# Performance work log

Hardware: AMD Instinct MI355X
Metric: run time of the kernel (lower is better)

## Reference

```python
import jax, jax.numpy as jnp
import numpy as np

N, C, H, W = 8, 256, 56, 56
DEPTH, HEADS, NWIN, TOPK, MLPR = 4, 8, 7, 4, 4
EPS = 1e-6


def setup_inputs() -> dict:
    key = jax.random.key(0)
    ks = jax.random.split(key, 16)
    s = 0.02
    return {
        'x': jax.random.normal(ks[0], (N, C, H, W), jnp.float32),
        'ln1_w': jnp.ones((DEPTH, C), jnp.float32),
        'ln1_b': jnp.zeros((DEPTH, C), jnp.float32),
        'qkv_w': jax.random.normal(ks[1], (DEPTH, C, 3 * C), jnp.float32) * s,
        'qkv_b': jnp.zeros((DEPTH, 3 * C), jnp.float32),
        'lepe_w': jax.random.normal(ks[2], (DEPTH, C, 1, 5, 5), jnp.float32) * s,
        'lepe_b': jnp.zeros((DEPTH, C), jnp.float32),
        'wo_w': jax.random.normal(ks[3], (DEPTH, C, C), jnp.float32) * s,
        'wo_b': jnp.zeros((DEPTH, C), jnp.float32),
        'ln2_w': jnp.ones((DEPTH, C), jnp.float32),
        'ln2_b': jnp.zeros((DEPTH, C), jnp.float32),
        'mlp1_w': jax.random.normal(ks[4], (DEPTH, C, MLPR * C), jnp.float32) * s,
        'mlp1_b': jnp.zeros((DEPTH, MLPR * C), jnp.float32),
        'mlp2_w': jax.random.normal(ks[5], (DEPTH, MLPR * C, C), jnp.float32) * s,
        'mlp2_b': jnp.zeros((DEPTH, C), jnp.float32),
        'cse1_w': jax.random.normal(ks[6], (C // 16, C), jnp.float32) * s,
        'cse1_b': jnp.zeros((C // 16,), jnp.float32),
        'cse2_w': jax.random.normal(ks[7], (C, C // 16), jnp.float32) * s,
        'cse2_b': jnp.zeros((C,), jnp.float32),
        'sse_w': jax.random.normal(ks[8], (C, C), jnp.float32) * s,
        'sse_b': jnp.zeros((C,), jnp.float32),
        'conv_w': jax.random.normal(ks[9], (C, C, 3, 3), jnp.float32) * s,
        'conv_b': jnp.zeros((C,), jnp.float32),
    }


def _layernorm(x, w, b):
    mu = x.mean(-1, keepdims=True)
    var = ((x - mu) ** 2).mean(-1, keepdims=True)
    return (x - mu) * jax.lax.rsqrt(var + EPS) * w + b


def _dwconv5(x_nchw, k, b):
    # depthwise 5x5 conv, padding 2; k: (C,1,5,5)
    y = jax.lax.conv_general_dilated(
        x_nchw, k, (1, 1), [(2, 2), (2, 2)],
        dimension_numbers=('NCHW', 'OIHW', 'NCHW'), feature_group_count=C)
    return y + b[None, :, None, None]


def _bra(xn, qkv_w, qkv_b, lepe_w, lepe_b, wo_w, wo_b):
    # Bi-level routing attention on NHWC input (already layer-normed).
    j = NWIN; hh = H // j; ww = W // j; p2 = j * j; hw = hh * ww
    scale = C ** -0.5  # qk_dim == dim
    qkv = xn @ qkv_w + qkv_b                      # [N,H,W,3C]
    q, k, v = jnp.split(qkv, 3, axis=-1)

    def to_regions(t):  # [N,H,W,C] -> [N,p2,hw,C]
        return t.reshape(N, j, hh, j, ww, C).transpose(0, 1, 3, 2, 4, 5).reshape(N, p2, hw, C)

    q_pix, k_pix, v_pix = to_regions(q), to_regions(k), to_regions(v)
    # region-level descriptors (routing is detached in original: diff_routing=False)
    q_win = jax.lax.stop_gradient(q_pix.mean(2))  # [N,p2,C]
    k_win = jax.lax.stop_gradient(k_pix.mean(2))
    logits = jnp.einsum('npc,nqc->npq', q_win * scale, k_win)
    _, idx = jax.lax.top_k(logits, TOPK)          # [N,p2,TOPK]; routing weights unused (mul_weight='none')
    bidx = jnp.arange(N)[:, None, None]
    k_sel = k_pix[bidx, idx]                      # [N,p2,TOPK,hw,C] irregular gather
    v_sel = v_pix[bidx, idx]
    m = HEADS; cd = C // m
    qh = q_pix.reshape(N, p2, hw, m, cd)
    kh = k_sel.reshape(N, p2, TOPK * hw, m, cd)
    vh = v_sel.reshape(N, p2, TOPK * hw, m, cd)
    attn = jnp.einsum('npqmc,npkmc->npmqk', qh * scale, kh)
    attn = jax.nn.softmax(attn, axis=-1)
    out = jnp.einsum('npmqk,npkmc->npqmc', attn, vh).reshape(N, p2, hw, C)
    out = out.reshape(N, j, j, hh, ww, C).transpose(0, 1, 3, 2, 4, 5).reshape(N, H, W, C)
    lepe = _dwconv5(v.transpose(0, 3, 1, 2), lepe_w, lepe_b).transpose(0, 2, 3, 1)
    return (out + lepe) @ wo_w + wo_b


def _forward(x, ln1_w, ln1_b, qkv_w, qkv_b, lepe_w, lepe_b, wo_w, wo_b,
             ln2_w, ln2_b, mlp1_w, mlp1_b, mlp2_w, mlp2_b,
             cse1_w, cse1_b, cse2_w, cse2_b, sse_w, sse_b, conv_w, conv_b):
    xh = x.transpose(0, 2, 3, 1)  # NCHW -> NHWC
    for i in range(DEPTH):
        xh = xh + _bra(_layernorm(xh, ln1_w[i], ln1_b[i]),
                       qkv_w[i], qkv_b[i], lepe_w[i], lepe_b[i], wo_w[i], wo_b[i])
        xn = _layernorm(xh, ln2_w[i], ln2_b[i])
        h = jax.nn.gelu(xn @ mlp1_w[i] + mlp1_b[i], approximate=False)
        xh = xh + h @ mlp2_w[i] + mlp2_b[i]
    y = xh.transpose(0, 3, 1, 2)  # NHWC -> NCHW
    # SCSE gating
    pooled = y.mean((2, 3))  # [N,C] adaptive avg pool
    c = jax.nn.relu(pooled @ cse1_w.T + cse1_b)
    c = jax.nn.sigmoid(c @ cse2_w.T + cse2_b)  # [N,C]
    s = jax.nn.sigmoid(jnp.einsum('nchw,oc->nohw', y, sse_w) + sse_b[None, :, None, None])
    y = y * c[:, :, None, None] + y * s
    # final 3x3 conv, padding 1
    y = jax.lax.conv_general_dilated(
        y, conv_w, (1, 1), [(1, 1), (1, 1)],
        dimension_numbers=('NCHW', 'OIHW', 'NCHW')) + conv_b[None, :, None, None]
    return y


def reference(x, ln1_w, ln1_b, qkv_w, qkv_b, lepe_w, lepe_b, wo_w, wo_b,
              ln2_w, ln2_b, mlp1_w, mlp1_b, mlp2_w, mlp2_b,
              cse1_w, cse1_b, cse2_w, cse2_b, sse_w, sse_b, conv_w, conv_b):
    return _forward(x, ln1_w, ln1_b, qkv_w, qkv_b, lepe_w, lepe_b, wo_w, wo_b,
                    ln2_w, ln2_b, mlp1_w, mlp1_b, mlp2_w, mlp2_b,
                    cse1_w, cse1_b, cse2_w, cse2_b, sse_w, sse_b, conv_w, conv_b)
```

## Files before the change

kernel.cpp:

```cpp
#include <hip/hip_runtime.h>

#define PIX 25088
#define NB 8
#define HH 56
#define WW 56
#define CC 256
#define P2 49
#define TOPKN 4

typedef short s16x8 __attribute__((ext_vector_type(8)));
typedef float f32x4 __attribute__((ext_vector_type(4)));

__device__ __forceinline__ float gelu_f(float v){
    return 0.5f*v*(1.0f+erff(v*0.70710678118654752f));
}
__device__ __forceinline__ float sigmoid_f(float v){
    return 1.0f/(1.0f+__expf(-v));
}
__device__ __forceinline__ unsigned short f2bf(float f){
    union { float f; unsigned u; } x; x.f = f;
    unsigned r = x.u + 0x7fffu + ((x.u >> 16) & 1u);
    return (unsigned short)(r >> 16);
}
__device__ __forceinline__ float bf2f(unsigned short u){
    union { unsigned u; float f; } x; x.u = ((unsigned)u) << 16; return x.f;
}
__device__ __forceinline__ void gload_lds16(const void* g, void* l){
    __builtin_amdgcn_global_load_lds((const __attribute__((address_space(1))) void*)g,
                                     (__attribute__((address_space(3))) void*)l, 16, 0, 0);
}

__global__ __launch_bounds__(1024) void nchw_to_nhwc(const float* __restrict__ in, float* __restrict__ out){
    __shared__ float t[32][33];
    int pb = blockIdx.x;
    int n  = pb / 98;
    int p0 = (pb % 98) * 32;
    int c0 = blockIdx.y * 32;
    int tx = threadIdx.x, ty = threadIdx.y;
    t[ty][tx] = in[(size_t)(n*CC + c0+ty)*3136 + p0 + tx];
    __syncthreads();
    out[(size_t)(n*3136 + p0 + ty)*CC + c0 + tx] = t[tx][ty];
}

__global__ __launch_bounds__(1024) void wtrans(const float* __restrict__ in, unsigned short* __restrict__ out,
                                               int K, int N){
    int layer = blockIdx.z;
    in  += (size_t)layer*K*N;
    out += (size_t)layer*K*N;
    __shared__ float t[32][33];
    int n0 = blockIdx.x*32, k0 = blockIdx.y*32;
    t[threadIdx.y][threadIdx.x] = in[(size_t)(k0+threadIdx.y)*N + n0 + threadIdx.x];
    __syncthreads();
    out[(size_t)(n0+threadIdx.y)*K + k0 + threadIdx.x] = f2bf(t[threadIdx.x][threadIdx.y]);
}

__global__ __launch_bounds__(256) void tobf16(const float* __restrict__ in, unsigned short* __restrict__ out, int n){
    int i = blockIdx.x*256 + threadIdx.x;
    if(i < n) out[i] = f2bf(in[i]);
}

__global__ __launch_bounds__(256) void convw_reorder(const float* __restrict__ in, unsigned short* __restrict__ out){
    int idx = blockIdx.x*256 + threadIdx.x;
    if(idx >= 256*256*9) return;
    int o = idx / (256*9); int rem = idx % (256*9); int c = rem/9; int t = rem%9;
    out[(size_t)t*65536 + o*256 + c] = f2bf(in[idx]);
}

__global__ __launch_bounds__(256) void ln_bf16(const float* __restrict__ x, const float* __restrict__ w,
                                               const float* __restrict__ b, unsigned short* __restrict__ y){
    int row = blockIdx.x*4 + (threadIdx.x >> 6);
    int lane = threadIdx.x & 63;
    const float4 v = *reinterpret_cast<const float4*>(&x[(size_t)row*CC + lane*4]);
    float s = v.x + v.y + v.z + v.w;
    #pragma unroll
    for(int off=32; off>0; off>>=1) s += __shfl_xor(s, off);
    float mu = s*(1.0f/CC);
    float d0=v.x-mu, d1=v.y-mu, d2=v.z-mu, d3=v.w-mu;
    float sq = d0*d0 + d1*d1 + d2*d2 + d3*d3;
    #pragma unroll
    for(int off=32; off>0; off>>=1) sq += __shfl_xor(sq, off);
    float rs = rsqrtf(sq*(1.0f/CC) + 1e-6f);
    const float4 wv = *reinterpret_cast<const float4*>(&w[lane*4]);
    const float4 bv = *reinterpret_cast<const float4*>(&b[lane*4]);
    ushort4 o;
    o.x = f2bf(d0*rs*wv.x + bv.x);
    o.y = f2bf(d1*rs*wv.y + bv.y);
    o.z = f2bf(d2*rs*wv.z + bv.z);
    o.w = f2bf(d3*rs*wv.w + bv.w);
    *reinterpret_cast<ushort4*>(&y[(size_t)row*CC + lane*4]) = o;
}

template<int EPI, bool HASRES, bool OUTF, bool OUTB>
__global__ __launch_bounds__(256) void mfma_gemm(
    const unsigned short* __restrict__ A, const unsigned short* __restrict__ Bt,
    const float* __restrict__ bias, const float* __restrict__ res,
    float* __restrict__ Cf, unsigned short* __restrict__ Cb,
    int M, int N, int K)
{
    __shared__ __align__(16) unsigned short As[4096];
    __shared__ __align__(16) unsigned short Bs[4096];
    const int tid = threadIdx.x;
    const int wid = tid >> 6, lane = tid & 63;
    const int row0 = blockIdx.y << 7, col0 = blockIdx.x << 7;
    const int wm = wid >> 1, wn = wid & 1;
    const int li = lane & 15, qq = lane >> 4;

    f32x4 acc[4][4] = {};
    const int nk = K >> 5;
    for(int kt=0; kt<nk; kt++){
        const int k0 = kt << 5;
        #pragma unroll
        for(int i=0;i<2;i++){
            int boff = wid*2048 + i*1024 + (lane<<4);
            int row = boff >> 6;
            int t = (boff >> 4) & 3;
            int q = t ^ ((row >> 1) & 3);
            gload_lds16(A  + (size_t)(row0+row)*K + k0 + q*8, (char*)As + wid*2048 + i*1024);
            gload_lds16(Bt + (size_t)(col0+row)*K + k0 + q*8, (char*)Bs + wid*2048 + i*1024);
        }
        __syncthreads();
        s16x8 af[4], bfr[4];
        #pragma unroll
        for(int mi=0;mi<4;mi++){
            int r = (wm<<6) + (mi<<4) + li;
            af[mi] = *(const s16x8*)((const char*)As + r*64 + ((qq ^ ((r>>1)&3))<<4));
        }
        #pragma unroll
        for(int nj=0;nj<4;nj++){
            int r = (wn<<6) + (nj<<4) + li;
            bfr[nj] = *(const s16x8*)((const char*)Bs + r*64 + ((qq ^ ((r>>1)&3))<<4));
        }
        #pragma unroll
        for(int mi=0;mi<4;mi++)
            #pragma unroll
            for(int nj=0;nj<4;nj++)
                acc[mi][nj] = __builtin_amdgcn_mfma_f32_16x16x32_bf16(af[mi], bfr[nj], acc[mi][nj], 0,0,0);
        __syncthreads();
    }
    #pragma unroll
    for(int mi=0;mi<4;mi++){
        #pragma unroll
        for(int nj=0;nj<4;nj++){
            int col = col0 + (wn<<6) + (nj<<4) + li;
            float bv = bias ? bias[col] : 0.0f;
            #pragma unroll
            for(int rr=0;rr<4;rr++){
                int row = row0 + (wm<<6) + (mi<<4) + (qq<<2) + rr;
                float v = acc[mi][nj][rr] + bv;
                if(EPI==1) v = gelu_f(v);
                if(EPI==2) v = sigmoid_f(v);
                if(HASRES) v += res[(size_t)row*N + col];
                if(OUTF) Cf[(size_t)row*N + col] = v;
                if(OUTB) Cb[(size_t)row*N + col] = f2bf(v);
            }
        }
    }
}

__global__ __launch_bounds__(256) void conv_gemm(
    const unsigned short* __restrict__ P, const unsigned short* __restrict__ CBt,
    const float* __restrict__ bias, float* __restrict__ out)
{
    __shared__ __align__(16) unsigned short As[4096];
    __shared__ __align__(16) unsigned short Bs[4096];
    const int tid = threadIdx.x;
    const int wid = tid >> 6, lane = tid & 63;
    const int row0 = blockIdx.y << 7, col0 = blockIdx.x << 7;
    const int wm = wid >> 1, wn = wid & 1;
    const int li = lane & 15, qq = lane >> 4;
    const int K = 256;

    f32x4 acc[4][4] = {};
    for(int tap=0; tap<9; tap++){
        int d = ((tap/3)-1)*58 + (tap%3) - 1;
        const unsigned short* A  = P + (size_t)(64 + d)*256;
        const unsigned short* Bt = CBt + (size_t)tap*65536;
        for(int kt=0; kt<8; kt++){
            const int k0 = kt << 5;
            #pragma unroll
            for(int i=0;i<2;i++){
                int boff = wid*2048 + i*1024 + (lane<<4);
                int row = boff >> 6;
                int t = (boff >> 4) & 3;
                int q = t ^ ((row >> 1) & 3);
                gload_lds16(A  + (size_t)(row0+row)*K + k0 + q*8, (char*)As + wid*2048 + i*1024);
                gload_lds16(Bt + (size_t)(col0+row)*K + k0 + q*8, (char*)Bs + wid*2048 + i*1024);
            }
            __syncthreads();
            s16x8 af[4], bfr[4];
            #pragma unroll
            for(int mi=0;mi<4;mi++){
                int r = (wm<<6) + (mi<<4) + li;
                af[mi] = *(const s16x8*)((const char*)As + r*64 + ((qq ^ ((r>>1)&3))<<4));
            }
            #pragma unroll
            for(int nj=0;nj<4;nj++){
                int r = (wn<<6) + (nj<<4) + li;
                bfr[nj] = *(const s16x8*)((const char*)Bs + r*64 + ((qq ^ ((r>>1)&3))<<4));
            }
            #pragma unroll
            for(int mi=0;mi<4;mi++)
                #pragma unroll
                for(int nj=0;nj<4;nj++)
                    acc[mi][nj] = __builtin_amdgcn_mfma_f32_16x16x32_bf16(af[mi], bfr[nj], acc[mi][nj], 0,0,0);
            __syncthreads();
        }
    }
    #pragma unroll
    for(int mi=0;mi<4;mi++){
        #pragma unroll
        for(int nj=0;nj<4;nj++){
            int col = col0 + (wn<<6) + (nj<<4) + li;
            float bv = bias[col];
            #pragma unroll
            for(int rr=0;rr<4;rr++){
                int prow = row0 + (wm<<6) + (mi<<4) + (qq<<2) + rr;
                if(prow < NB*3364){
                    int n = prow / 3364; int rem = prow % 3364;
                    int y = rem / 58, x = rem % 58;
                    if(y>=1 && y<57 && x>=1 && x<57){
                        out[(((size_t)n*CC + col)*HH + (y-1))*WW + (x-1)] = acc[mi][nj][rr] + bv;
                    }
                }
            }
        }
    }
}

__global__ __launch_bounds__(256) void winmean_kernel(const float* __restrict__ qkv,
                                                      float* __restrict__ qwin, float* __restrict__ kwin){
    int b = blockIdx.x;
    int n = b / P2, p = b % P2;
    int c = threadIdx.x;
    int hb = (p/7)*8, wb = (p%7)*8;
    float sq=0.f, sk=0.f;
    for(int pixi=0;pixi<64;pixi++){
        int h = hb + (pixi>>3), w = wb + (pixi&7);
        const float* row = &qkv[((size_t)(n*HH+h)*WW + w)*768];
        sq += row[c];
        sk += row[256+c];
    }
    qwin[(size_t)b*CC+c] = sq*(1.0f/64.0f);
    kwin[(size_t)b*CC+c] = sk*(1.0f/64.0f);
}

__global__ __launch_bounds__(64) void route_kernel(const float* __restrict__ qwin, const float* __restrict__ kwin,
                                                   int* __restrict__ idxout){
    int b = blockIdx.x;
    int n = b / P2;
    int j = threadIdx.x;
    __shared__ float lg[64];
    float v = -1e30f;
    if(j < P2){
        const float* q = &qwin[(size_t)b*CC];
        const float* k = &kwin[(size_t)(n*P2+j)*CC];
        float s=0.f;
        for(int c=0;c<CC;c++) s += q[c]*k[c];
        v = s*0.0625f;
    }
    lg[j] = v;
    __syncthreads();
    if(j==0){
        for(int t=0;t<TOPKN;t++){
            int best=0; float bv=lg[0];
            for(int u=1;u<P2;u++) if(lg[u]>bv){bv=lg[u];best=u;}
            idxout[b*TOPKN+t]=best;
            lg[best]=-1e30f;
        }
    }
}

__global__ __launch_bounds__(64) void attn_kernel(const float* __restrict__ qkv, const int* __restrict__ idx,
                                                  float* __restrict__ out){
    __shared__ __align__(16) unsigned short P_lds[64*32];
    __shared__ int pixo[256];
    int b = blockIdx.x;
    int m = b & 7; int np = b >> 3;
    int n = np / P2, p = np % P2;
    int lane = threadIdx.x;
    int li = lane & 15, g = lane >> 4;
    int hb = (p/7)*8, wb = (p%7)*8;

    #pragma unroll
    for(int t4=0;t4<4;t4++){
        int r = idx[np*TOPKN + t4];
        int pixi = lane;
        int h = (r/7)*8 + (pixi>>3), w = (r%7)*8 + (pixi&7);
        pixo[t4*64 + lane] = (n*HH+h)*WW + w;
    }
    __syncthreads();

    const float QS = 0.0625f * 1.44269504088896f;
    s16x8 qfr[4];
    #pragma unroll
    for(int q4=0;q4<4;q4++){
        int q = q4*16 + li;
        int h = hb + (q>>3), w = wb + (q&7);
        const float* qr = &qkv[((size_t)(n*HH+h)*WW + w)*768 + m*32 + g*8];
        s16x8 f;
        #pragma unroll
        for(int j=0;j<8;j++) f[j] = (short)f2bf(qr[j]*QS);
        qfr[q4] = f;
    }

    f32x4 ot[2][4] = {};
    float mx[4], lsum[4];
    #pragma unroll
    for(int q4=0;q4<4;q4++){ mx[q4] = -3e38f; lsum[q4] = 0.0f; }

    for(int kb=0; kb<8; kb++){
        f32x4 st[2][4] = {};
        #pragma unroll
        for(int kf=0;kf<2;kf++){
            int key = kb*32 + kf*16 + li;
            const float* kr = &qkv[(size_t)pixo[key]*768 + 256 + m*32 + g*8];
            s16x8 kfrag;
            #pragma unroll
            for(int j=0;j<8;j++) kfrag[j] = (short)f2bf(kr[j]);
            #pragma unroll
            for(int q4=0;q4<4;q4++)
                st[kf][q4] = __builtin_amdgcn_mfma_f32_16x16x32_bf16(kfrag, qfr[q4], st[kf][q4], 0,0,0);
        }
        #pragma unroll
        for(int q4=0;q4<4;q4++){
            float pm = st[0][q4][0];
            #pragma unroll
            for(int r=1;r<4;r++) pm = fmaxf(pm, st[0][q4][r]);
            #pragma unroll
            for(int r=0;r<4;r++) pm = fmaxf(pm, st[1][q4][r]);
            pm = fmaxf(pm, __shfl_xor(pm, 16));
            pm = fmaxf(pm, __shfl_xor(pm, 32));
            float mnew = fmaxf(mx[q4], pm);
            float fsc = exp2f(mx[q4] - mnew);
            mx[q4] = mnew;
            float ps = 0.0f;
            #pragma unroll
            for(int kf=0;kf<2;kf++)
                #pragma unroll
                for(int r=0;r<4;r++){
                    float pv = exp2f(st[kf][q4][r] - mnew);
                    st[kf][q4][r] = pv;
                    ps += pv;
                }
            ps += __shfl_xor(ps, 16);
            ps += __shfl_xor(ps, 32);
            lsum[q4] = lsum[q4]*fsc + ps;
            #pragma unroll
            for(int chf=0;chf<2;chf++)
                #pragma unroll
                for(int r=0;r<4;r++) ot[chf][q4][r] *= fsc;
        }
        #pragma unroll
        for(int q4=0;q4<4;q4++){
            int q = q4*16 + li;
            #pragma unroll
            for(int kf=0;kf<2;kf++){
                unsigned lo = ((unsigned)f2bf(st[kf][q4][0])) | (((unsigned)f2bf(st[kf][q4][1]))<<16);
                unsigned hi = ((unsigned)f2bf(st[kf][q4][2])) | (((unsigned)f2bf(st[kf][q4][3]))<<16);
                int byte = (q*64 + kf*32 + g*8) ^ ((q&3)<<4);
                *reinterpret_cast<uint2*>((char*)P_lds + byte) = make_uint2(lo, hi);
            }
        }
        __syncthreads();
        s16x8 pfr[4];
        #pragma unroll
        for(int q4=0;q4<4;q4++){
            int q = q4*16 + li;
            int byte = (q*64 + g*16) ^ ((q&3)<<4);
            pfr[q4] = *reinterpret_cast<const s16x8*>((const char*)P_lds + byte);
        }
        #pragma unroll
        for(int chf=0;chf<2;chf++){
            s16x8 vfr;
            #pragma unroll
            for(int j=0;j<8;j++){
                int key = kb*32 + g*8 + j;
                vfr[j] = (short)f2bf(qkv[(size_t)pixo[key]*768 + 512 + m*32 + chf*16 + li]);
            }
            #pragma unroll
            for(int q4=0;q4<4;q4++)
                ot[chf][q4] = __builtin_amdgcn_mfma_f32_16x16x32_bf16(vfr, pfr[q4], ot[chf][q4], 0,0,0);
        }
        __syncthreads();
    }
    #pragma unroll
    for(int q4=0;q4<4;q4++){
        int q = q4*16 + li;
        int h = hb + (q>>3), w = wb + (q&7);
        float inv = 1.0f / lsum[q4];
        float* orow = &out[((size_t)(n*HH+h)*WW + w)*CC + m*32];
        #pragma unroll
        for(int chf=0;chf<2;chf++)
            #pragma unroll
            for(int r=0;r<4;r++)
                orow[chf*16 + g*4 + r] = ot[chf][q4][r]*inv;
    }
}

__global__ __launch_bounds__(256) void lepe_kernel(const float* __restrict__ qkv, const float* __restrict__ attn,
                                                   const float* __restrict__ lw, const float* __restrict__ lb,
                                                   unsigned short* __restrict__ outb){
    __shared__ float tile[144][64];
    int tileid = blockIdx.x;
    int cg = blockIdx.y;
    int n = blockIdx.z;
    int hb = (tileid/7)*8, wb = (tileid%7)*8;
    int tid = threadIdx.x;
    for(int ii=tid; ii<144*64; ii+=256){
        int sp = ii >> 6, cl = ii & 63;
        int ty = sp / 12, tx = sp % 12;
        int y = hb + ty - 2, x = wb + tx - 2;
        float v = 0.0f;
        if(y>=0 && y<HH && x>=0 && x<WW)
            v = qkv[((size_t)(n*HH+y)*WW + x)*768 + 512 + cg*64 + cl];
        tile[sp][cl] = v;
    }
    __syncthreads();
    int cl = tid & 63;
    int c = cg*64 + cl;
    float wv[25];
    #pragma unroll
    for(int t=0;t<25;t++) wv[t] = lw[c*25 + t];
    float bias = lb[c];
    for(int oi = tid; oi < 4096; oi += 256){
        int sp = oi >> 6;
        int py = sp >> 3, px = sp & 7;
        float a = bias;
        #pragma unroll
        for(int dy=0;dy<5;dy++)
            #pragma unroll
            for(int dx=0;dx<5;dx++)
                a += tile[(py+dy)*12 + px+dx][cl]*wv[dy*5+dx];
        size_t pix = (size_t)(n*HH + hb+py)*WW + wb+px;
        outb[pix*CC + c] = f2bf(attn[pix*CC + c] + a);
    }
}

__global__ __launch_bounds__(256) void pool_kernel(const float* __restrict__ x, float* __restrict__ pooled){
    int n = blockIdx.x, c = threadIdx.x;
    float s=0.f;
    for(int p=0;p<3136;p++) s += x[((size_t)n*3136+p)*CC + c];
    pooled[n*CC+c] = s*(1.0f/3136.0f);
}

__global__ __launch_bounds__(256) void cse_kernel(const float* __restrict__ pooled,
                                                  const float* __restrict__ w1, const float* __restrict__ b1,
                                                  const float* __restrict__ w2, const float* __restrict__ b2,
                                                  float* __restrict__ cfac){
    int n = blockIdx.x, t = threadIdx.x;
    __shared__ float c1[16];
    if(t < 16){
        float s = b1[t];
        for(int c=0;c<CC;c++) s += pooled[n*CC+c]*w1[t*CC+c];
        c1[t] = fmaxf(s, 0.0f);
    }
    __syncthreads();
    float s = b2[t];
    #pragma unroll
    for(int j=0;j<16;j++) s += c1[j]*w2[t*16+j];
    cfac[n*CC+t] = sigmoid_f(s);
}

__global__ __launch_bounds__(256) void gate_pad(const float* __restrict__ x, const float* __restrict__ s,
                                                const float* __restrict__ cfac, unsigned short* __restrict__ P){
    int pix = blockIdx.x;
    int n = pix / 3136; int rem = pix % 3136; int h = rem/56, w = rem%56;
    int c = threadIdx.x;
    float v = x[(size_t)pix*CC + c]*(cfac[n*CC+c] + s[(size_t)pix*CC + c]);
    size_t q = 64 + (size_t)n*3364 + (size_t)(h+1)*58 + (w+1);
    P[q*CC + c] = f2bf(v);
}

extern "C" void kernel_launch(void* const* d_in, const int* in_sizes, int n_in,
                              void* d_out, int out_size, void* d_ws, size_t ws_size,
                              hipStream_t stream){
    const float* x_in   = (const float*)d_in[0];
    const float* ln1w   = (const float*)d_in[1];
    const float* ln1b   = (const float*)d_in[2];
    const float* qkvw   = (const float*)d_in[3];
    const float* qkvb   = (const float*)d_in[4];
    const float* lepew  = (const float*)d_in[5];
    const float* lepeb  = (const float*)d_in[6];
    const float* wow    = (const float*)d_in[7];
    const float* wob    = (const float*)d_in[8];
    const float* ln2w   = (const float*)d_in[9];
    const float* ln2b   = (const float*)d_in[10];
    const float* mlp1w  = (const float*)d_in[11];
    const float* mlp1b  = (const float*)d_in[12];
    const float* mlp2w  = (const float*)d_in[13];
    const float* mlp2b  = (const float*)d_in[14];
    const float* cse1w  = (const float*)d_in[15];
    const float* cse1b  = (const float*)d_in[16];
    const float* cse2w  = (const float*)d_in[17];
    const float* cse2b  = (const float*)d_in[18];
    const float* ssew   = (const float*)d_in[19];
    const float* sseb   = (const float*)d_in[20];
    const float* convw  = (const float*)d_in[21];
    const float* convb  = (const float*)d_in[22];
    float* out = (float*)d_out;

    float* ws     = (float*)d_ws;
    float* bufx   = ws;
    float* buftmp = bufx   + (size_t)PIX*CC;
    float* bufqkv = buftmp + (size_t)PIX*CC;
    float* qwin   = bufqkv + (size_t)PIX*768;
    float* kwin   = qwin + (size_t)NB*P2*CC;
    float* pooled = kwin + (size_t)NB*P2*CC;
    float* cfac   = pooled + NB*CC;
    int*   idxb   = (int*)(cfac + NB*CC);
    unsigned short* bufxn = (unsigned short*)(cfac + NB*CC + 2048);
    unsigned short* qkvbt = bufxn + (size_t)PIX*CC;
    unsigned short* wobt  = qkvbt + (size_t)4*768*256;
    unsigned short* m1bt  = wobt  + (size_t)4*256*256;
    unsigned short* m2bt  = m1bt  + (size_t)4*1024*256;
    unsigned short* ssebt = m2bt  + (size_t)4*256*1024;
    unsigned short* cvbt  = ssebt + (size_t)256*256;

    unsigned short* Ppad = (unsigned short*)bufqkv;
    unsigned short* hid  = (unsigned short*)bufqkv;

    wtrans<<<dim3(24, 8, 4), dim3(32,32), 0, stream>>>(qkvw, qkvbt, 256, 768);
    wtrans<<<dim3(8, 8, 4),  dim3(32,32), 0, stream>>>(wow,  wobt,  256, 256);
    wtrans<<<dim3(32, 8, 4), dim3(32,32), 0, stream>>>(mlp1w, m1bt, 256, 1024);
    wtrans<<<dim3(8, 32, 4), dim3(32,32), 0, stream>>>(mlp2w, m2bt, 1024, 256);
    tobf16<<<256, 256, 0, stream>>>(ssew, ssebt, 65536);
    convw_reorder<<<2304, 256, 0, stream>>>(convw, cvbt);

    nchw_to_nhwc<<<dim3(NB*98, 8), dim3(32,32), 0, stream>>>(x_in, bufx);

    for(int i=0;i<4;i++){
        ln_bf16<<<PIX/4,256,0,stream>>>(bufx, ln1w+i*CC, ln1b+i*CC, bufxn);
        mfma_gemm<0,false,true,false><<<dim3(6,196),256,0,stream>>>(
            bufxn, qkvbt+(size_t)i*768*256, qkvb+i*768, nullptr, bufqkv, nullptr, PIX, 768, 256);
        winmean_kernel<<<NB*P2,256,0,stream>>>(bufqkv, qwin, kwin);
        route_kernel<<<NB*P2,64,0,stream>>>(qwin, kwin, idxb);
        attn_kernel<<<NB*P2*8,64,0,stream>>>(bufqkv, idxb, buftmp);
        lepe_kernel<<<dim3(49,4,NB),256,0,stream>>>(bufqkv, buftmp, lepew+(size_t)i*CC*25, lepeb+i*CC, bufxn);
        mfma_gemm<0,true,true,false><<<dim3(2,196),256,0,stream>>>(
            bufxn, wobt+(size_t)i*256*256, wob+i*CC, bufx, bufx, nullptr, PIX, 256, 256);
        ln_bf16<<<PIX/4,256,0,stream>>>(bufx, ln2w+i*CC, ln2b+i*CC, bufxn);
        mfma_gemm<1,false,false,true><<<dim3(8,196),256,0,stream>>>(
            bufxn, m1bt+(size_t)i*1024*256, mlp1b+i*1024, nullptr, nullptr, hid, PIX, 1024, 256);
        mfma_gemm<0,true,true,false><<<dim3(2,196),256,0,stream>>>(
            hid, m2bt+(size_t)i*256*1024, mlp2b+i*CC, bufx, bufx, nullptr, PIX, 256, 1024);
    }

    pool_kernel<<<NB,256,0,stream>>>(bufx, pooled);
    cse_kernel<<<NB,256,0,stream>>>(pooled, cse1w, cse1b, cse2w, cse2b, cfac);
    tobf16<<<PIX,256,0,stream>>>(bufx, bufxn, PIX*CC);
    mfma_gemm<2,false,true,false><<<dim3(2,196),256,0,stream>>>(
        bufxn, ssebt, sseb, nullptr, buftmp, nullptr, PIX, 256, 256);
    hipMemsetAsync(Ppad, 0, (size_t)27136*256*2, stream);
    gate_pad<<<PIX,256,0,stream>>>(bufx, buftmp, cfac, Ppad);
    conv_gemm<<<dim3(2,211),256,0,stream>>>(Ppad, cvbt, convb, out);
}
```

Measured before the change: 1.382 ms.

## Store QKV in bf16, fuse SSE gating into GEMM, parallelize pooling

```diff
diff --git a/kernel.cpp b/kernel.cpp
--- a/kernel.cpp
+++ b/kernel.cpp
@@ -94,6 +94,7 @@
 __global__ __launch_bounds__(256) void mfma_gemm(
     const unsigned short* __restrict__ A, const unsigned short* __restrict__ Bt,
     const float* __restrict__ bias, const float* __restrict__ res,
+    const float* __restrict__ gfac,
     float* __restrict__ Cf, unsigned short* __restrict__ Cb,
     int M, int N, int K)
 {
@@ -149,9 +150,18 @@
                 float v = acc[mi][nj][rr] + bv;
                 if(EPI==1) v = gelu_f(v);
                 if(EPI==2) v = sigmoid_f(v);
-                if(HASRES) v += res[(size_t)row*N + col];
-                if(OUTF) Cf[(size_t)row*N + col] = v;
-                if(OUTB) Cb[(size_t)row*N + col] = f2bf(v);
+                if(EPI==3){
+                    int n = row / 3136; int rem = row % 3136;
+                    int h = rem / 56, w = rem % 56;
+                    float xv = res[(size_t)row*N + col];
+                    v = xv*(gfac[n*CC + col] + sigmoid_f(v));
+                    size_t dst = ((size_t)(64 + n*3364 + (h+1)*58 + (w+1)))*CC + col;
+                    Cb[dst] = f2bf(v);
+                } else {
+                    if(HASRES) v += res[(size_t)row*N + col];
+                    if(OUTF) Cf[(size_t)row*N + col] = v;
+                    if(OUTB) Cb[(size_t)row*N + col] = f2bf(v);
+                }
             }
         }
     }
@@ -227,7 +237,7 @@
     }
 }
 
-__global__ __launch_bounds__(256) void winmean_kernel(const float* __restrict__ qkv,
+__global__ __launch_bounds__(256) void winmean_kernel(const unsigned short* __restrict__ qkv,
                                                       float* __restrict__ qwin, float* __restrict__ kwin){
     int b = blockIdx.x;
     int n = b / P2, p = b % P2;
@@ -236,9 +246,9 @@
     float sq=0.f, sk=0.f;
     for(int pixi=0;pixi<64;pixi++){
         int h = hb + (pixi>>3), w = wb + (pixi&7);
-        const float* row = &qkv[((size_t)(n*HH+h)*WW + w)*768];
-        sq += row[c];
-        sk += row[256+c];
+        const unsigned short* row = &qkv[((size_t)(n*HH+h)*WW + w)*768];
+        sq += bf2f(row[c]);
+        sk += bf2f(row[256+c]);
     }
     qwin[(size_t)b*CC+c] = sq*(1.0f/64.0f);
     kwin[(size_t)b*CC+c] = sk*(1.0f/64.0f);
@@ -270,7 +280,8 @@
     }
 }
 
-__global__ __launch_bounds__(64) void attn_kernel(const float* __restrict__ qkv, const int* __restrict__ idx,
+__global__ __launch_bounds__(64) void attn_kernel(const unsigned short* __restrict__ qkv,
+                                                  const int* __restrict__ idx,
                                                   float* __restrict__ out){
     __shared__ __align__(16) unsigned short P_lds[64*32];
     __shared__ int pixo[256];
@@ -290,19 +301,15 @@
     }
     __syncthreads();
 
-    const float QS = 0.0625f * 1.44269504088896f;
     s16x8 qfr[4];
     #pragma unroll
     for(int q4=0;q4<4;q4++){
         int q = q4*16 + li;
         int h = hb + (q>>3), w = wb + (q&7);
-        const float* qr = &qkv[((size_t)(n*HH+h)*WW + w)*768 + m*32 + g*8];
-        s16x8 f;
-        #pragma unroll
-        for(int j=0;j<8;j++) f[j] = (short)f2bf(qr[j]*QS);
-        qfr[q4] = f;
-    }
-
+        qfr[q4] = *reinterpret_cast<const s16x8*>(&qkv[((size_t)(n*HH+h)*WW + w)*768 + m*32 + g*8]);
+    }
+
+    const float SC = 0.0625f * 1.44269504088896f;
     f32x4 ot[2][4] = {};
     float mx[4], lsum[4];
     #pragma unroll
@@ -313,14 +320,17 @@
         #pragma unroll
         for(int kf=0;kf<2;kf++){
             int key = kb*32 + kf*16 + li;
-            const float* kr = &qkv[(size_t)pixo[key]*768 + 256 + m*32 + g*8];
-            s16x8 kfrag;
-            #pragma unroll
-            for(int j=0;j<8;j++) kfrag[j] = (short)f2bf(kr[j]);
+            s16x8 kfrag = *reinterpret_cast<const s16x8*>(&qkv[(size_t)pixo[key]*768 + 256 + m*32 + g*8]);
             #pragma unroll
             for(int q4=0;q4<4;q4++)
                 st[kf][q4] = __builtin_amdgcn_mfma_f32_16x16x32_bf16(kfrag, qfr[q4], st[kf][q4], 0,0,0);
         }
+        #pragma unroll
+        for(int kf=0;kf<2;kf++)
+            #pragma unroll
+            for(int q4=0;q4<4;q4++)
+                #pragma unroll
+                for(int r=0;r<4;r++) st[kf][q4][r] *= SC;
         #pragma unroll
         for(int q4=0;q4<4;q4++){
             float pm = st[0][q4][0];
@@ -375,7 +385,7 @@
             #pragma unroll
             for(int j=0;j<8;j++){
                 int key = kb*32 + g*8 + j;
-                vfr[j] = (short)f2bf(qkv[(size_t)pixo[key]*768 + 512 + m*32 + chf*16 + li]);
+                vfr[j] = (short)qkv[(size_t)pixo[key]*768 + 512 + m*32 + chf*16 + li];
             }
             #pragma unroll
             for(int q4=0;q4<4;q4++)
@@ -397,7 +407,8 @@
     }
 }
 
-__global__ __launch_bounds__(256) void lepe_kernel(const float* __restrict__ qkv, const float* __restrict__ attn,
+__global__ __launch_bounds__(256) void lepe_kernel(const unsigned short* __restrict__ qkv,
+                                                   const float* __restrict__ attn,
                                                    const float* __restrict__ lw, const float* __restrict__ lb,
                                                    unsigned short* __restrict__ outb){
     __shared__ float tile[144][64];
@@ -412,7 +423,7 @@
         int y = hb + ty - 2, x = wb + tx - 2;
         float v = 0.0f;
         if(y>=0 && y<HH && x>=0 && x<WW)
-            v = qkv[((size_t)(n*HH+y)*WW + x)*768 + 512 + cg*64 + cl];
+            v = bf2f(qkv[((size_t)(n*HH+y)*WW + x)*768 + 512 + cg*64 + cl]);
         tile[sp][cl] = v;
     }
     __syncthreads();
@@ -437,10 +448,11 @@
 }
 
 __global__ __launch_bounds__(256) void pool_kernel(const float* __restrict__ x, float* __restrict__ pooled){
-    int n = blockIdx.x, c = threadIdx.x;
+    int n = blockIdx.y, c = threadIdx.x;
+    int p0 = blockIdx.x*64;
     float s=0.f;
-    for(int p=0;p<3136;p++) s += x[((size_t)n*3136+p)*CC + c];
-    pooled[n*CC+c] = s*(1.0f/3136.0f);
+    for(int pp=0;pp<64;pp++) s += x[((size_t)n*3136 + p0 + pp)*CC + c];
+    atomicAdd(&pooled[n*CC+c], s*(1.0f/3136.0f));
 }
 
 __global__ __launch_bounds__(256) void cse_kernel(const float* __restrict__ pooled,
@@ -459,16 +471,6 @@
     #pragma unroll
     for(int j=0;j<16;j++) s += c1[j]*w2[t*16+j];
     cfac[n*CC+t] = sigmoid_f(s);
-}
-
-__global__ __launch_bounds__(256) void gate_pad(const float* __restrict__ x, const float* __restrict__ s,
-                                                const float* __restrict__ cfac, unsigned short* __restrict__ P){
-    int pix = blockIdx.x;
-    int n = pix / 3136; int rem = pix % 3136; int h = rem/56, w = rem%56;
-    int c = threadIdx.x;
-    float v = x[(size_t)pix*CC + c]*(cfac[n*CC+c] + s[(size_t)pix*CC + c]);
-    size_t q = 64 + (size_t)n*3364 + (size_t)(h+1)*58 + (w+1);
-    P[q*CC + c] = f2bf(v);
 }
 
 extern "C" void kernel_launch(void* const* d_in, const int* in_sizes, int n_in,
@@ -499,25 +501,24 @@
     const float* convb  = (const float*)d_in[22];
     float* out = (float*)d_out;
 
-    float* ws     = (float*)d_ws;
-    float* bufx   = ws;
-    float* buftmp = bufx   + (size_t)PIX*CC;
-    float* bufqkv = buftmp + (size_t)PIX*CC;
-    float* qwin   = bufqkv + (size_t)PIX*768;
-    float* kwin   = qwin + (size_t)NB*P2*CC;
-    float* pooled = kwin + (size_t)NB*P2*CC;
-    float* cfac   = pooled + NB*CC;
-    int*   idxb   = (int*)(cfac + NB*CC);
-    unsigned short* bufxn = (unsigned short*)(cfac + NB*CC + 2048);
-    unsigned short* qkvbt = bufxn + (size_t)PIX*CC;
-    unsigned short* wobt  = qkvbt + (size_t)4*768*256;
-    unsigned short* m1bt  = wobt  + (size_t)4*256*256;
-    unsigned short* m2bt  = m1bt  + (size_t)4*1024*256;
-    unsigned short* ssebt = m2bt  + (size_t)4*256*1024;
-    unsigned short* cvbt  = ssebt + (size_t)256*256;
-
-    unsigned short* Ppad = (unsigned short*)bufqkv;
-    unsigned short* hid  = (unsigned short*)bufqkv;
+    char* base = (char*)d_ws;
+    float* bufx   = (float*)base;                         base += (size_t)PIX*CC*4;
+    float* buftmp = (float*)base;                         base += (size_t)PIX*CC*4;
+    unsigned short* qkvB = (unsigned short*)base;
+    unsigned short* hid  = (unsigned short*)base;
+    unsigned short* Ppad = (unsigned short*)base;         base += (size_t)PIX*1024*2;
+    float* qwin   = (float*)base;                         base += (size_t)NB*P2*CC*4;
+    float* kwin   = (float*)base;                         base += (size_t)NB*P2*CC*4;
+    float* pooled = (float*)base;                         base += NB*CC*4;
+    float* cfac   = (float*)base;                         base += NB*CC*4;
+    int*   idxb   = (int*)base;                           base += 2048*4;
+    unsigned short* bufxn = (unsigned short*)base;        base += (size_t)PIX*CC*2;
+    unsigned short* qkvbt = (unsigned short*)base;        base += (size_t)4*768*256*2;
+    unsigned short* wobt  = (unsigned short*)base;        base += (size_t)4*256*256*2;
+    unsigned short* m1bt  = (unsigned short*)base;        base += (size_t)4*1024*256*2;
+    unsigned short* m2bt  = (unsigned short*)base;        base += (size_t)4*256*1024*2;
+    unsigned short* ssebt = (unsigned short*)base;        base += (size_t)256*256*2;
+    unsigned short* cvbt  = (unsigned short*)base;        base += (size_t)9*256*256*2;
 
     wtrans<<<dim3(24, 8, 4), dim3(32,32), 0, stream>>>(qkvw, qkvbt, 256, 768);
     wtrans<<<dim3(8, 8, 4),  dim3(32,32), 0, stream>>>(wow,  wobt,  256, 256);
@@ -530,27 +531,27 @@
 
     for(int i=0;i<4;i++){
         ln_bf16<<<PIX/4,256,0,stream>>>(bufx, ln1w+i*CC, ln1b+i*CC, bufxn);
-        mfma_gemm<0,false,true,false><<<dim3(6,196),256,0,stream>>>(
-            bufxn, qkvbt+(size_t)i*768*256, qkvb+i*768, nullptr, bufqkv, nullptr, PIX, 768, 256);
-        winmean_kernel<<<NB*P2,256,0,stream>>>(bufqkv, qwin, kwin);
+        mfma_gemm<0,false,false,true><<<dim3(6,196),256,0,stream>>>(
+            bufxn, qkvbt+(size_t)i*768*256, qkvb+i*768, nullptr, nullptr, nullptr, qkvB, PIX, 768, 256);
+        winmean_kernel<<<NB*P2,256,0,stream>>>(qkvB, qwin, kwin);
         route_kernel<<<NB*P2,64,0,stream>>>(qwin, kwin, idxb);
-        attn_kernel<<<NB*P2*8,64,0,stream>>>(bufqkv, idxb, buftmp);
-        lepe_kernel<<<dim3(49,4,NB),256,0,stream>>>(bufqkv, buftmp, lepew+(size_t)i*CC*25, lepeb+i*CC, bufxn);
+        attn_kernel<<<NB*P2*8,64,0,stream>>>(qkvB, idxb, buftmp);
+        lepe_kernel<<<dim3(49,4,NB),256,0,stream>>>(qkvB, buftmp, lepew+(size_t)i*CC*25, lepeb+i*CC, bufxn);
         mfma_gemm<0,true,true,false><<<dim3(2,196),256,0,stream>>>(
-            bufxn, wobt+(size_t)i*256*256, wob+i*CC, bufx, bufx, nullptr, PIX, 256, 256);
+            bufxn, wobt+(size_t)i*256*256, wob+i*CC, bufx, nullptr, bufx, nullptr, PIX, 256, 256);
         ln_bf16<<<PIX/4,256,0,stream>>>(bufx, ln2w+i*CC, ln2b+i*CC, bufxn);
         mfma_gemm<1,false,false,true><<<dim3(8,196),256,0,stream>>>(
-            bufxn, m1bt+(size_t)i*1024*256, mlp1b+i*1024, nullptr, nullptr, hid, PIX, 1024, 256);
+            bufxn, m1bt+(size_t)i*1024*256, mlp1b+i*1024, nullptr, nullptr, nullptr, hid, PIX, 1024, 256);
         mfma_gemm<0,true,true,false><<<dim3(2,196),256,0,stream>>>(
-            hid, m2bt+(size_t)i*256*1024, mlp2b+i*CC, bufx, bufx, nullptr, PIX, 256, 1024);
-    }
-
-    pool_kernel<<<NB,256,0,stream>>>(bufx, pooled);
+            hid, m2bt+(size_t)i*256*1024, mlp2b+i*CC, bufx, nullptr, bufx, nullptr, PIX, 256, 1024);
+    }
+
+    hipMemsetAsync(pooled, 0, NB*CC*sizeof(float), stream);
+    pool_kernel<<<dim3(49,NB),256,0,stream>>>(bufx, pooled);
     cse_kernel<<<NB,256,0,stream>>>(pooled, cse1w, cse1b, cse2w, cse2b, cfac);
     tobf16<<<PIX,256,0,stream>>>(bufx, bufxn, PIX*CC);
-    mfma_gemm<2,false,true,false><<<dim3(2,196),256,0,stream>>>(
-        bufxn, ssebt, sseb, nullptr, buftmp, nullptr, PIX, 256, 256);
     hipMemsetAsync(Ppad, 0, (size_t)27136*256*2, stream);
-    gate_pad<<<PIX,256,0,stream>>>(bufx, buftmp, cfac, Ppad);
+    mfma_gemm<3,false,false,false><<<dim3(2,196),256,0,stream>>>(
+        bufxn, ssebt, sseb, bufx, cfac, nullptr, Ppad, PIX, 256, 256);
     conv_gemm<<<dim3(2,211),256,0,stream>>>(Ppad, cvbt, convb, out);
 }
```

Result: faster. 1.283 ms (-7.2%).
